# Kernel optimization log

Hardware: AMD Instinct MI355X
Metric: run time of the kernel (lower is better)

## Reference

```python
import jax, jax.numpy as jnp
import numpy as np

B = 4096
F_ST, F_DY, M = 20, 10, 50
E = 16
N_ST, N_DY = 100000, 1000000
F_ALL = F_ST + F_DY                      # 30 fields total
P = F_ALL * (F_ALL - 1) // 2             # 435 strict upper-triangular pairs
D_IN = P * E                             # 6960 MLP input dim
H = 512
BN_EPS = 1e-5


def _bn(x, g, b):
    # BatchNorm1d in training mode: biased batch variance (matches torch)
    m = jnp.mean(x, axis=0)
    v = jnp.var(x, axis=0)
    return g * (x - m) * jax.lax.rsqrt(v + BN_EPS) + b


def setup_inputs() -> dict:
    key = jax.random.key(0)
    ks = jax.random.split(key, 16)
    s_emb = 0.02
    inp = {
        "static_ids": jax.random.randint(ks[0], (B, F_ST), 0, N_ST),
        "dynamic_ids": jax.random.randint(ks[1], (B, F_DY, M), 0, N_DY),
        "dynamic_lengths": jax.random.randint(ks[2], (B, F_DY), 1, M + 1),
        "st_emb": jax.random.normal(ks[3], (N_ST, E), jnp.float32) * s_emb,
        "dy_emb": jax.random.normal(ks[4], (N_DY, E), jnp.float32) * s_emb,
        "st_lr": jax.random.normal(ks[5], (N_ST, 1), jnp.float32) * s_emb,
        "dy_lr": jax.random.normal(ks[6], (N_DY, 1), jnp.float32) * s_emb,
        "bias": jax.random.normal(ks[7], (1,), jnp.float32),
        "bn1_g": jnp.ones((D_IN,), jnp.float32), "bn1_b": jnp.zeros((D_IN,), jnp.float32),
        "W1": jax.random.normal(ks[8], (D_IN, H), jnp.float32) / np.sqrt(D_IN),
        "b1": jnp.zeros((H,), jnp.float32),
        "bn2_g": jnp.ones((H,), jnp.float32), "bn2_b": jnp.zeros((H,), jnp.float32),
        "W2": jax.random.normal(ks[9], (H, H), jnp.float32) / np.sqrt(H),
        "b2": jnp.zeros((H,), jnp.float32),
        "bn3_g": jnp.ones((H,), jnp.float32), "bn3_b": jnp.zeros((H,), jnp.float32),
        "W3": jax.random.normal(ks[10], (H, H), jnp.float32) / np.sqrt(H),
        "b3": jnp.zeros((H,), jnp.float32),
        "bn_out_g": jnp.ones((H,), jnp.float32), "bn_out_b": jnp.zeros((H,), jnp.float32),
        "W_out": jax.random.normal(ks[11], (H, 1), jnp.float32) / np.sqrt(H),
        "b_out": jnp.zeros((1,), jnp.float32),
    }
    return inp


def reference(static_ids, dynamic_ids, dynamic_lengths,
              st_emb, dy_emb, st_lr, dy_lr, bias,
              bn1_g, bn1_b, W1, b1,
              bn2_g, bn2_b, W2, b2,
              bn3_g, bn3_b, W3, b3,
              bn_out_g, bn_out_b, W_out, b_out):
    lengths = jnp.maximum(dynamic_lengths, 1)                       # guard avg div
    valid = (jnp.arange(M)[None, None, :] < lengths[:, :, None])    # [B,Fdy,M]
    valid_f = valid.astype(jnp.float32)

    # DyEmb (method='avg'): masked mean over list positions -> [B,Fdy,E]
    dyn_tab = dy_emb[dynamic_ids]                                   # [B,Fdy,M,E]
    dyn_embeddings = jnp.einsum('bfme,bfm->bfe', dyn_tab, valid_f) / lengths[..., None].astype(jnp.float32)
    # StEmb: plain lookup -> [B,Fst,E]
    st_embeddings = st_emb[static_ids]

    all_emb = jnp.concatenate([st_embeddings, dyn_embeddings], axis=1)  # [B,F_ALL,E]

    # Strict upper triangle pairs (static indices == the boolean mask in torch code)
    iu, ju = np.triu_indices(F_ALL, k=1)                            # each [P]
    combine = all_emb[:, iu, :] * all_emb[:, ju, :]                 # [B,P,E]
    x = combine.reshape(combine.shape[0], -1)                       # [B, P*E]

    # Linear parts: StEmb/DyEmb with embedding_size=1 (dyLr uses method='sum')
    static_lr_out = st_lr[static_ids][..., 0]                       # [B,Fst]
    dyn_lr_out = jnp.einsum('bfm,bfm->bf', dy_lr[dynamic_ids][..., 0], valid_f)  # [B,Fdy]

    # BN -> Linear -> ReLU tower
    h1 = _bn(x, bn1_g, bn1_b) @ W1 + b1
    h2 = _bn(jax.nn.relu(h1), bn2_g, bn2_b) @ W2 + b2
    out3 = _bn(jax.nn.relu(h2), bn3_g, bn3_b) @ W3 + b3             # embedding_lr_out_3
    # final BN+Linear is computed in torch but unused in scores (kept faithful)
    _ = _bn(jax.nn.relu(out3), bn_out_g, bn_out_b) @ W_out + b_out

    scores = (bias
              + jnp.sum(static_lr_out, axis=-1)
              + jnp.sum(dyn_lr_out, axis=-1)
              + jnp.sum(out3, axis=-1))                             # [B]
    return scores
```

## Files before the change

kernel.cpp:

```cpp
#include <hip/hip_runtime.h>

typedef __attribute__((ext_vector_type(8))) short short8;
typedef __attribute__((ext_vector_type(4))) float f32x4;

__device__ __forceinline__ unsigned short f2b(float f) {
    union { float f; unsigned u; } uf; uf.f = f;
    unsigned r = uf.u + 0x7fffu + ((uf.u >> 16) & 1u);
    return (unsigned short)(r >> 16);
}
__device__ __forceinline__ float b2f(unsigned short b) {
    union { unsigned u; float f; } uf; uf.u = ((unsigned)b) << 16;
    return uf.f;
}
__device__ __forceinline__ void gload_lds16(const void* g, void* l) {
    __builtin_amdgcn_global_load_lds(
        (const __attribute__((address_space(1))) void*)g,
        (__attribute__((address_space(3))) void*)l,
        16, 0, 0);
}

#define B_SZ 4096
#define F_ST 20
#define F_DY 10
#define MLEN 50
#define E_SZ 16
#define F_ALL 30
#define NPAIR 435
#define DIN 6960
#define KP 7168
#define H_SZ 512
#define BN_EPS 1e-5f

__global__ __launch_bounds__(256) void k_stemb(
    const int* __restrict__ st_ids, const float* __restrict__ st_emb,
    float* __restrict__ all_emb)
{
    int idx = blockIdx.x * 256 + threadIdx.x;
    int e4 = idx & 3, bf = idx >> 2;
    int b = bf / F_ST, f = bf % F_ST;
    int id = st_ids[bf];
    f32x4 v = *(const f32x4*)(st_emb + (long)id * E_SZ + e4 * 4);
    *(f32x4*)(all_emb + ((long)b * F_ALL + f) * E_SZ + e4 * 4) = v;
}

__global__ __launch_bounds__(512) void k_dyemb(
    const int* __restrict__ dy_ids, const int* __restrict__ dy_len,
    const float* __restrict__ dy_emb, float* __restrict__ all_emb)
{
    int gw = blockIdx.x * 8 + (threadIdx.x >> 6);
    int l = threadIdx.x & 63;
    int b = gw / F_DY, f = gw - b * F_DY;
    int len = dy_len[b * F_DY + f]; if (len < 1) len = 1;
    const int* ids = dy_ids + ((long)b * F_DY + f) * MLEN;
    int idv = (l < MLEN) ? ids[l] : 0;
    int e = l & 15, mq = l >> 4;
    float acc = 0.f;
#pragma unroll
    for (int j = 0; j < 13; ++j) {
        int m = mq + (j << 2);
        int id = __shfl(idv, m, 64);
        float v = (m < len) ? dy_emb[(long)id * E_SZ + e] : 0.f;
        acc += v;
    }
    acc += __shfl_xor(acc, 16, 64);
    acc += __shfl_xor(acc, 32, 64);
    if (l < 16)
        all_emb[((long)b * F_ALL + F_ST + f) * E_SZ + e] = acc / (float)len;
}

__global__ __launch_bounds__(512) void k_lr(
    const int* __restrict__ st_ids, const int* __restrict__ dy_ids,
    const int* __restrict__ dy_len, const float* __restrict__ st_lr,
    const float* __restrict__ dy_lr, const float* __restrict__ bias,
    float* __restrict__ lr_score)
{
    int w = threadIdx.x >> 6, l = threadIdx.x & 63;
    int b = blockIdx.x * 8 + w;
    float acc = 0.f;
    if (l < F_ST) acc += st_lr[st_ids[b * F_ST + l]];
#pragma unroll
    for (int i = 0; i < 8; ++i) {
        int idx = i * 64 + l;
        if (idx < F_DY * MLEN) {
            int f = idx / MLEN, m = idx - f * MLEN;
            int len = dy_len[b * F_DY + f]; if (len < 1) len = 1;
            if (m < len)
                acc += dy_lr[dy_ids[((long)b * F_DY + f) * MLEN + m]];
        }
    }
    for (int s = 32; s; s >>= 1) acc += __shfl_down(acc, s, 64);
    if (l == 0) lr_score[b] = bias[0] + acc;
}

__global__ __launch_bounds__(256) void k_x(
    const float* __restrict__ all_emb, unsigned short* __restrict__ x16,
    float* __restrict__ s1, float* __restrict__ s1q)
{
    __shared__ float es[16 * 480];
    __shared__ int pip[NPAIR], pjp[NPAIR];
    int t = threadIdx.x, b0 = blockIdx.x * 16;
    for (int p = t; p < NPAIR; p += 256) {
        int i = 0, rem = p;
        while (rem >= (F_ALL - 1) - i) { rem -= (F_ALL - 1) - i; ++i; }
        pip[p] = i; pjp[p] = i + 1 + rem;
    }
    for (int idx = t; idx < 16 * 480; idx += 256)
        es[idx] = all_emb[(long)b0 * 480 + idx];
    __syncthreads();

    int ci[28], cj[28];
#pragma unroll
    for (int k = 0; k < 28; ++k) {
        int d = t + (k << 8);
        if (d < DIN) {
            int p = d >> 4, e = d & 15;
            ci[k] = pip[p] * E_SZ + e;
            cj[k] = pjp[p] * E_SZ + e;
        } else { ci[k] = -1; cj[k] = 0; }
    }
    float sum[28], sq[28];
#pragma unroll
    for (int k = 0; k < 28; ++k) { sum[k] = 0.f; sq[k] = 0.f; }

    for (int r = 0; r < 16; ++r) {
        const float* row = &es[r * 480];
        long ob = (long)(b0 + r) * KP;
#pragma unroll
        for (int k = 0; k < 28; ++k) {
            int d = t + (k << 8);
            if (ci[k] >= 0) {
                float v = row[ci[k]] * row[cj[k]];
                unsigned short h = f2b(v);
                x16[ob + d] = h;
                float vb = b2f(h);
                sum[k] += vb; sq[k] += vb * vb;
            } else {
                x16[ob + d] = 0;
            }
        }
    }
#pragma unroll
    for (int k = 0; k < 28; ++k) {
        int d = t + (k << 8);
        if (ci[k] >= 0) { atomicAdd(&s1[d], sum[k]); atomicAdd(&s1q[d], sq[k]); }
    }
}

__global__ __launch_bounds__(256) void k_prep(
    const float* __restrict__ s, const float* __restrict__ sqs,
    const float* __restrict__ g, const float* __restrict__ bb,
    float* __restrict__ a, float* __restrict__ c,
    const float* __restrict__ W3, float* __restrict__ w3s)
{
    int t = threadIdx.x;
    if (blockIdx.x < 28) {
        int d = blockIdx.x * 256 + t;
        if (d < DIN) {
            float m = s[d] * (1.f / 4096.f);
            float var = sqs[d] * (1.f / 4096.f) - m * m;
            float av = g[d] * rsqrtf(var + BN_EPS);
            a[d] = av; c[d] = bb[d] - m * av;
        }
    } else {
        int row = (blockIdx.x - 28) * 16 + (t >> 4), sub = t & 15;
        float acc = 0.f;
        for (int i = 0; i < 32; ++i) acc += W3[(long)row * H_SZ + sub + i * 16];
#pragma unroll
        for (int sh = 8; sh; sh >>= 1) acc += __shfl_xor(acc, sh, 16);
        if (sub == 0) w3s[row] = acc;
    }
}

__global__ __launch_bounds__(256) void k_w1t(
    const float* __restrict__ W1, const float* __restrict__ a1,
    const float* __restrict__ c1, unsigned short* __restrict__ w1t,
    float* __restrict__ con)
{
    int gi = blockIdx.x * 256 + threadIdx.x;
    int kg = gi >> 9, n = gi & 511;
    short8 out; float cacc = 0.f;
#pragma unroll
    for (int i = 0; i < 8; ++i) {
        int k = kg * 8 + i;
        if (k < DIN) {
            float w = W1[(long)k * H_SZ + n];
            out[i] = (short)f2b(a1[k] * w);
            cacc += c1[k] * w;
        } else out[i] = 0;
    }
    *(short8*)(w1t + (long)n * KP + kg * 8) = out;
    atomicAdd(&con[n], cacc);
}

__global__ __launch_bounds__(512, 2) void k_gemm1(
    const unsigned short* __restrict__ A, const unsigned short* __restrict__ Bt,
    float* __restrict__ accbuf)
{
    __shared__ __align__(16) short As[2][128 * 64];
    __shared__ __align__(16) short Bs[2][512 * 64];
    const int t = threadIdx.x;
    const int w = t >> 6, l = t & 63;
    const int lm = l & 15, lq = l >> 4;
    const int s = blockIdx.x;
    const int row0 = (s >> 3) * 128;
    const int k0 = (s & 7) * (KP / 8);

    const int srow = t >> 3;
    const int gch = (t & 7) ^ (srow & 7);
    const unsigned short* gA = A + (long)(row0 + srow) * KP + k0 + gch * 8;
    const unsigned short* gB = Bt + (long)srow * KP + k0 + gch * 8;

    f32x4 acc[8][4];
#pragma unroll
    for (int mi = 0; mi < 8; ++mi)
#pragma unroll
        for (int ni = 0; ni < 4; ++ni) acc[mi][ni] = (f32x4){0.f,0.f,0.f,0.f};

#define STAGE1(kt, pb) do {                                                   \
        const unsigned short* a_ = gA + (kt) * 64;                            \
        const unsigned short* b_ = gB + (kt) * 64;                            \
        gload_lds16(a_, &As[pb][w * 512]);                   \
        gload_lds16(a_ + (long)64 * KP, &As[pb][4096 + w * 512]); \
        _Pragma("unroll")                                                     \
        for (int c_ = 0; c_ < 8; ++c_)                       \
            gload_lds16(b_ + (long)(64 * c_) * KP, &Bs[pb][c_ * 4096 + w * 512]); \
    } while (0)

    STAGE1(0, 0);
    __syncthreads();

    for (int kt = 0; kt < 14; ++kt) {
        const int pb = kt & 1;
        if (kt < 13) STAGE1(kt + 1, pb ^ 1);
#pragma unroll
        for (int sb = 0; sb < 2; ++sb) {
            short8 af[8];
#pragma unroll
            for (int mi = 0; mi < 8; ++mi) {
                int m = mi * 16 + lm;
                int sl = (sb * 4 + lq) ^ (m & 7);
                af[mi] = *(const short8*)(&As[pb][m * 64 + sl * 8]);
            }
#pragma unroll
            for (int ni = 0; ni < 4; ++ni) {
                int rb = w * 64 + ni * 16 + lm;
                int sl = (sb * 4 + lq) ^ (rb & 7);
                short8 bf = *(const short8*)(&Bs[pb][rb * 64 + sl * 8]);
#pragma unroll
                for (int mi = 0; mi < 8; ++mi)
                    acc[mi][ni] = __builtin_amdgcn_mfma_f32_16x16x32_bf16(
                        af[mi], bf, acc[mi][ni], 0, 0, 0);
            }
        }
        __syncthreads();
    }

#pragma unroll
    for (int ni = 0; ni < 4; ++ni) {
        int col = w * 64 + ni * 16 + lm;
#pragma unroll
        for (int mi = 0; mi < 8; ++mi) {
            int rbase = row0 + mi * 16 + lq * 4;
#pragma unroll
            for (int r = 0; r < 4; ++r)
                atomicAdd(&accbuf[(long)(rbase + r) * H_SZ + col], acc[mi][ni][r]);
        }
    }
#undef STAGE1
}

__global__ __launch_bounds__(256) void k_ep(
    const float* __restrict__ accbuf, const float* __restrict__ con1,
    const float* __restrict__ b1, unsigned short* __restrict__ r1,
    float* __restrict__ s2, float* __restrict__ s2q)
{
    __shared__ float con[H_SZ];
    int t = threadIdx.x, r0 = blockIdx.x * 32;
    con[t] = b1[t] + con1[t];
    con[t + 256] = b1[t + 256] + con1[t + 256];
    __syncthreads();
    float a0 = 0.f, q0 = 0.f, a1v = 0.f, q1 = 0.f;
    for (int r = 0; r < 32; ++r) {
        long base = (long)(r0 + r) * H_SZ;
        float v0 = accbuf[base + t] + con[t];
        float v1 = accbuf[base + t + 256] + con[t + 256];
        v0 = v0 > 0.f ? v0 : 0.f;
        v1 = v1 > 0.f ? v1 : 0.f;
        unsigned short h0 = f2b(v0), h1 = f2b(v1);
        r1[base + t] = h0; r1[base + t + 256] = h1;
        float b0 = b2f(h0), b1f = b2f(h1);
        a0 += b0; q0 += b0 * b0; a1v += b1f; q1 += b1f * b1f;
    }
    atomicAdd(&s2[t], a0);        atomicAdd(&s2q[t], q0);
    atomicAdd(&s2[t + 256], a1v); atomicAdd(&s2q[t + 256], q1);
}

__global__ __launch_bounds__(256) void k_w2t(
    const float* __restrict__ W2, const float* __restrict__ s2,
    const float* __restrict__ s2q, const float* __restrict__ g2,
    const float* __restrict__ bb2, unsigned short* __restrict__ w2t,
    float* __restrict__ con)
{
    int gi = blockIdx.x * 256 + threadIdx.x;
    int kg = gi >> 9, n = gi & 511;
    short8 out; float cacc = 0.f;
#pragma unroll
    for (int i = 0; i < 8; ++i) {
        int k = kg * 8 + i;
        float m = s2[k] * (1.f / 4096.f);
        float var = s2q[k] * (1.f / 4096.f) - m * m;
        float av = g2[k] * rsqrtf(var + BN_EPS);
        float cv = bb2[k] - m * av;
        float w = W2[(long)k * H_SZ + n];
        out[i] = (short)f2b(av * w);
        cacc += cv * w;
    }
    *(short8*)(w2t + (long)n * H_SZ + kg * 8) = out;
    atomicAdd(&con[n], cacc);
}

__global__ __launch_bounds__(512) void k_gemm2(
    const unsigned short* __restrict__ A, const unsigned short* __restrict__ Bt,
    const float* __restrict__ cvec, const float* __restrict__ bvec,
    unsigned short* __restrict__ Out, float* __restrict__ ss,
    float* __restrict__ sq)
{
    const int Kp = H_SZ;
    __shared__ __align__(16) short As[2][128 * 32];
    __shared__ __align__(16) short Bs[2][64 * 32];
    const int t = threadIdx.x;
    const int w = t >> 6, l = t & 63;
    const int wm = w >> 1, wn = w & 1;
    const int lm = l & 15, lq = l >> 4;
    const int row0 = blockIdx.y * 128;
    const int col0 = blockIdx.x * 64;

    const unsigned short* gA = A + (long)(row0 + (t >> 2)) * Kp + ((t & 3) * 8);
    const unsigned short* gB = Bt + (long)(col0 + ((t >> 2) & 63)) * Kp + ((t & 3) * 8);

#define STAGE2(kt, pb) do {                                                   \
        gload_lds16(gA + (kt) * 32, &As[pb][w * 512]);                        \
        if (t < 256) gload_lds16(gB + (kt) * 32, &Bs[pb][w * 512]);           \
    } while (0)

    f32x4 acc00 = {0.f,0.f,0.f,0.f}, acc01 = acc00, acc10 = acc00, acc11 = acc00;

    STAGE2(0, 0);
    __syncthreads();

    for (int kt = 0; kt < Kp / 32; ++kt) {
        const int pb = kt & 1;
        if (kt < Kp / 32 - 1) STAGE2(kt + 1, pb ^ 1);
        const short* aBase0 = &As[pb][(wm * 32 + lm) * 32 + lq * 8];
        const short* bBase0 = &Bs[pb][(wn * 32 + lm) * 32 + lq * 8];
        short8 af0 = *(const short8*)aBase0;
        short8 af1 = *(const short8*)(aBase0 + 16 * 32);
        short8 bf0 = *(const short8*)bBase0;
        short8 bf1 = *(const short8*)(bBase0 + 16 * 32);
        acc00 = __builtin_amdgcn_mfma_f32_16x16x32_bf16(af0, bf0, acc00, 0, 0, 0);
        acc01 = __builtin_amdgcn_mfma_f32_16x16x32_bf16(af0, bf1, acc01, 0, 0, 0);
        acc10 = __builtin_amdgcn_mfma_f32_16x16x32_bf16(af1, bf0, acc10, 0, 0, 0);
        acc11 = __builtin_amdgcn_mfma_f32_16x16x32_bf16(af1, bf1, acc11, 0, 0, 0);
        __syncthreads();
    }
#undef STAGE2

    f32x4 accs[2][2] = {{acc00, acc01}, {acc10, acc11}};
#pragma unroll
    for (int ni = 0; ni < 2; ++ni) {
        int col = col0 + wn * 32 + ni * 16 + lm;
        float cb = cvec[col] + bvec[col];
        float psum = 0.f, psq = 0.f;
#pragma unroll
        for (int mi = 0; mi < 2; ++mi) {
            int rbase = row0 + wm * 32 + mi * 16 + lq * 4;
#pragma unroll
            for (int r = 0; r < 4; ++r) {
                float v = accs[mi][ni][r] + cb;
                v = v > 0.f ? v : 0.f;
                unsigned short h = f2b(v);
                Out[(long)(rbase + r) * H_SZ + col] = h;
                float vb = b2f(h);
                psum += vb; psq += vb * vb;
            }
        }
        psum += __shfl_xor(psum, 16, 64); psum += __shfl_xor(psum, 32, 64);
        psq  += __shfl_xor(psq , 16, 64); psq  += __shfl_xor(psq , 32, 64);
        if (lq == 0) { atomicAdd(&ss[col], psum); atomicAdd(&sq[col], psq); }
    }
}

__global__ __launch_bounds__(256) void k_final(
    const unsigned short* __restrict__ r2, const float* __restrict__ s3,
    const float* __restrict__ s3q, const float* __restrict__ g3,
    const float* __restrict__ bb3, const float* __restrict__ w3s,
    const float* __restrict__ b3, const float* __restrict__ lr_score,
    float* __restrict__ out)
{
    int t = threadIdx.x, w = t >> 6, l = t & 63;
    int b = blockIdx.x * 4 + w;
    float acc = 0.f;
#pragma unroll
    for (int i = 0; i < 8; ++i) {
        int e = i * 64 + l;
        float m = s3[e] * (1.f / 4096.f);
        float var = s3q[e] * (1.f / 4096.f) - m * m;
        float a3 = g3[e] * rsqrtf(var + BN_EPS);
        float c3 = bb3[e] - m * a3;
        float v = a3 * b2f(r2[(long)b * H_SZ + e]) + c3;
        acc += v * w3s[e] + b3[e];
    }
    for (int s = 32; s; s >>= 1) acc += __shfl_down(acc, s, 64);
    if (l == 0) out[b] = lr_score[b] + acc;
}

extern "C" void kernel_launch(void* const* d_in, const int* in_sizes, int n_in,
                              void* d_out, int out_size, void* d_ws, size_t ws_size,
                              hipStream_t stream) {
    const int*   st_ids = (const int*)d_in[0];
    const int*   dy_ids = (const int*)d_in[1];
    const int*   dy_len = (const int*)d_in[2];
    const float* st_emb = (const float*)d_in[3];
    const float* dy_emb = (const float*)d_in[4];
    const float* st_lr  = (const float*)d_in[5];
    const float* dy_lr  = (const float*)d_in[6];
    const float* bias   = (const float*)d_in[7];
    const float* bn1_g  = (const float*)d_in[8];
    const float* bn1_b  = (const float*)d_in[9];
    const float* W1     = (const float*)d_in[10];
    const float* b1     = (const float*)d_in[11];
    const float* bn2_g  = (const float*)d_in[12];
    const float* bn2_b  = (const float*)d_in[13];
    const float* W2     = (const float*)d_in[14];
    const float* b2     = (const float*)d_in[15];
    const float* bn3_g  = (const float*)d_in[16];
    const float* bn3_b  = (const float*)d_in[17];
    const float* W3     = (const float*)d_in[18];
    const float* b3     = (const float*)d_in[19];

    char* ws = (char*)d_ws;
    size_t off = 0;
    auto alloc = [&](size_t bytes) -> char* {
        char* p = ws + off;
        off = (off + bytes + 255) & ~(size_t)255;
        return p;
    };
    char* R = alloc((size_t)B_SZ * H_SZ * 4);
    float*          all_emb = (float*)R;
    float*          accbuf  = (float*)R;
    unsigned short* r2      = (unsigned short*)R;

    unsigned short* x16     = (unsigned short*)alloc((size_t)B_SZ * KP * 2);
    unsigned short* w1t     = (unsigned short*)alloc((size_t)H_SZ * KP * 2);
    unsigned short* r1      = (unsigned short*)alloc((size_t)B_SZ * H_SZ * 2);
    unsigned short* w2t     = (unsigned short*)alloc((size_t)H_SZ * H_SZ * 2);
    float*          lr_sc   = (float*)alloc(B_SZ * 4);
    float* a1  = (float*)alloc(KP * 4);
    float* c1  = (float*)alloc(KP * 4);
    float* w3s = (float*)alloc(H_SZ * 4);
    char* zstart = ws + off;
    float* s1   = (float*)alloc(KP * 4);
    float* s1q  = (float*)alloc(KP * 4);
    float* con1 = (float*)alloc(H_SZ * 4);
    float* s2   = (float*)alloc(H_SZ * 4);
    float* s2q  = (float*)alloc(H_SZ * 4);
    float* con2 = (float*)alloc(H_SZ * 4);
    float* s3   = (float*)alloc(H_SZ * 4);
    float* s3q  = (float*)alloc(H_SZ * 4);
    size_t zbytes = (size_t)((ws + off) - zstart);

    hipMemsetAsync(zstart, 0, zbytes, stream);
    k_stemb<<<(B_SZ * F_ST * 4) / 256, 256, 0, stream>>>(st_ids, st_emb, all_emb);
    k_dyemb<<<(B_SZ * F_DY) / 8, 512, 0, stream>>>(dy_ids, dy_len, dy_emb, all_emb);
    k_lr<<<B_SZ / 8, 512, 0, stream>>>(st_ids, dy_ids, dy_len, st_lr, dy_lr,
                                       bias, lr_sc);
    k_x<<<B_SZ / 16, 256, 0, stream>>>(all_emb, x16, s1, s1q);
    hipMemsetAsync(R, 0, (size_t)B_SZ * H_SZ * 4, stream);
    k_prep<<<60, 256, 0, stream>>>(s1, s1q, bn1_g, bn1_b, a1, c1, W3, w3s);
    k_w1t<<<(896 * 512) / 256, 256, 0, stream>>>(W1, a1, c1, w1t, con1);
    k_gemm1<<<256, 512, 0, stream>>>(x16, w1t, accbuf);
    k_ep<<<128, 256, 0, stream>>>(accbuf, con1, b1, r1, s2, s2q);
    k_w2t<<<128, 256, 0, stream>>>(W2, s2, s2q, bn2_g, bn2_b, w2t, con2);
    k_gemm2<<<dim3(8, 32), 512, 0, stream>>>(r1, w2t, con2, b2, r2, s3, s3q);
    k_final<<<B_SZ / 4, 256, 0, stream>>>(r2, s3, s3q, bn3_g, bn3_b, w3s, b3,
                                          lr_sc, (float*)d_out);
}
```

Measured before the change: 396.2 us.

## Halve GEMM1 row tile and load B operand directly from global into registers

GEMM1 row tiles shrink from 128 to 64 rows and the grid doubles to 512 blocks. The weight (B) operand is no longer staged through LDS. Each wave now loads its MFMA B fragments straight from global memory into registers, so LDS drops to a small A double buffer and more blocks fit per CU. The trade-off is that B reuse across row tiles moves to the caches instead of LDS, global B loads are not prefetched ahead of the MFMAs, and there are twice as many atomic adds into accbuf.

```diff
diff --git a/kernel.cpp b/kernel.cpp
--- a/kernel.cpp
+++ b/kernel.cpp
@@ -192,64 +192,60 @@
     atomicAdd(&con[n], cacc);
 }
 
-__global__ __launch_bounds__(512, 2) void k_gemm1(
+__global__ __launch_bounds__(512, 4) void k_gemm1(
     const unsigned short* __restrict__ A, const unsigned short* __restrict__ Bt,
     float* __restrict__ accbuf)
 {
-    __shared__ __align__(16) short As[2][128 * 64];
-    __shared__ __align__(16) short Bs[2][512 * 64];
+    __shared__ __align__(16) short As[2][64 * 64];
     const int t = threadIdx.x;
     const int w = t >> 6, l = t & 63;
     const int lm = l & 15, lq = l >> 4;
     const int s = blockIdx.x;
-    const int row0 = (s >> 3) * 128;
+    const int row0 = (s >> 3) * 64;
     const int k0 = (s & 7) * (KP / 8);
 
     const int srow = t >> 3;
     const int gch = (t & 7) ^ (srow & 7);
     const unsigned short* gA = A + (long)(row0 + srow) * KP + k0 + gch * 8;
-    const unsigned short* gB = Bt + (long)srow * KP + k0 + gch * 8;
-
-    f32x4 acc[8][4];
-#pragma unroll
-    for (int mi = 0; mi < 8; ++mi)
+
+    const unsigned short* gB0 = Bt + (long)(w * 64 + lm) * KP + k0 + lq * 8;
+    const unsigned short* gB1 = gB0 + (long)16 * KP;
+    const unsigned short* gB2 = gB0 + (long)32 * KP;
+    const unsigned short* gB3 = gB0 + (long)48 * KP;
+
+    f32x4 acc[4][4];
+#pragma unroll
+    for (int mi = 0; mi < 4; ++mi)
 #pragma unroll
         for (int ni = 0; ni < 4; ++ni) acc[mi][ni] = (f32x4){0.f,0.f,0.f,0.f};
 
-#define STAGE1(kt, pb) do {                                                   \
-        const unsigned short* a_ = gA + (kt) * 64;                            \
-        const unsigned short* b_ = gB + (kt) * 64;                            \
-        gload_lds16(a_, &As[pb][w * 512]);                   \
-        gload_lds16(a_ + (long)64 * KP, &As[pb][4096 + w * 512]); \
-        _Pragma("unroll")                                                     \
-        for (int c_ = 0; c_ < 8; ++c_)                       \
-            gload_lds16(b_ + (long)(64 * c_) * KP, &Bs[pb][c_ * 4096 + w * 512]); \
-    } while (0)
-
-    STAGE1(0, 0);
+    gload_lds16(gA, &As[0][w * 512]);
     __syncthreads();
 
     for (int kt = 0; kt < 14; ++kt) {
         const int pb = kt & 1;
-        if (kt < 13) STAGE1(kt + 1, pb ^ 1);
+        if (kt < 13)
+            gload_lds16(gA + (kt + 1) * 64, &As[pb ^ 1][w * 512]);
 #pragma unroll
         for (int sb = 0; sb < 2; ++sb) {
-            short8 af[8];
-#pragma unroll
-            for (int mi = 0; mi < 8; ++mi) {
+            const int ko = kt * 64 + sb * 32;
+            short8 bf0 = *(const short8*)(gB0 + ko);
+            short8 bf1 = *(const short8*)(gB1 + ko);
+            short8 bf2 = *(const short8*)(gB2 + ko);
+            short8 bf3 = *(const short8*)(gB3 + ko);
+            short8 af[4];
+#pragma unroll
+            for (int mi = 0; mi < 4; ++mi) {
                 int m = mi * 16 + lm;
                 int sl = (sb * 4 + lq) ^ (m & 7);
                 af[mi] = *(const short8*)(&As[pb][m * 64 + sl * 8]);
             }
 #pragma unroll
-            for (int ni = 0; ni < 4; ++ni) {
-                int rb = w * 64 + ni * 16 + lm;
-                int sl = (sb * 4 + lq) ^ (rb & 7);
-                short8 bf = *(const short8*)(&Bs[pb][rb * 64 + sl * 8]);
-#pragma unroll
-                for (int mi = 0; mi < 8; ++mi)
-                    acc[mi][ni] = __builtin_amdgcn_mfma_f32_16x16x32_bf16(
-                        af[mi], bf, acc[mi][ni], 0, 0, 0);
+            for (int mi = 0; mi < 4; ++mi) {
+                acc[mi][0] = __builtin_amdgcn_mfma_f32_16x16x32_bf16(af[mi], bf0, acc[mi][0], 0, 0, 0);
+                acc[mi][1] = __builtin_amdgcn_mfma_f32_16x16x32_bf16(af[mi], bf1, acc[mi][1], 0, 0, 0);
+                acc[mi][2] = __builtin_amdgcn_mfma_f32_16x16x32_bf16(af[mi], bf2, acc[mi][2], 0, 0, 0);
+                acc[mi][3] = __builtin_amdgcn_mfma_f32_16x16x32_bf16(af[mi], bf3, acc[mi][3], 0, 0, 0);
             }
         }
         __syncthreads();
@@ -259,14 +255,13 @@
     for (int ni = 0; ni < 4; ++ni) {
         int col = w * 64 + ni * 16 + lm;
 #pragma unroll
-        for (int mi = 0; mi < 8; ++mi) {
+        for (int mi = 0; mi < 4; ++mi) {
             int rbase = row0 + mi * 16 + lq * 4;
 #pragma unroll
             for (int r = 0; r < 4; ++r)
                 atomicAdd(&accbuf[(long)(rbase + r) * H_SZ + col], acc[mi][ni][r]);
         }
     }
-#undef STAGE1
 }
 
 __global__ __launch_bounds__(256) void k_ep(
@@ -478,7 +473,7 @@
     hipMemsetAsync(R, 0, (size_t)B_SZ * H_SZ * 4, stream);
     k_prep<<<60, 256, 0, stream>>>(s1, s1q, bn1_g, bn1_b, a1, c1, W3, w3s);
     k_w1t<<<(896 * 512) / 256, 256, 0, stream>>>(W1, a1, c1, w1t, con1);
-    k_gemm1<<<256, 512, 0, stream>>>(x16, w1t, accbuf);
+    k_gemm1<<<512, 512, 0, stream>>>(x16, w1t, accbuf);
     k_ep<<<128, 256, 0, stream>>>(accbuf, con1, b1, r1, s2, s2q);
     k_w2t<<<128, 256, 0, stream>>>(W2, s2, s2q, bn2_g, bn2_b, w2t, con2);
     k_gemm2<<<dim3(8, 32), 512, 0, stream>>>(r1, w2t, con2, b2, r2, s3, s3q);
```

Measured after the change: 417.6 us. 5.4% more time.
